# Optimization experiments

Hardware: AMD Instinct MI355X
Metric: run time of the kernel (lower is better)

## Reference

```python
import jax, jax.numpy as jnp
import numpy as np

WINDOW_SIZE = 11
SIGMA = 1.5
C1 = 0.01 ** 2
C2 = 0.03 ** 2


def _gaussian_window(channels):
    coords = jnp.arange(WINDOW_SIZE, dtype=jnp.float32) - WINDOW_SIZE // 2
    g = jnp.exp(-coords ** 2 / (2.0 * SIGMA ** 2))
    g = g / g.sum()
    w2d = g[:, None] * g[None, :]                      # [K, K]
    # depthwise kernel: [out_ch=C, in_ch/groups=1, K, K]
    return jnp.broadcast_to(w2d[None, None], (channels, 1, WINDOW_SIZE, WINDOW_SIZE))


def _depthwise_conv(x, window):
    # x: [B, C, H, W]; grouped conv with feature_group_count = C, SAME padding
    C = x.shape[1]
    pad = WINDOW_SIZE // 2
    return jax.lax.conv_general_dilated(
        x, window,
        window_strides=(1, 1),
        padding=((pad, pad), (pad, pad)),
        dimension_numbers=("NCHW", "OIHW", "NCHW"),
        feature_group_count=C,
    )


def setup_inputs() -> dict:
    key = jax.random.key(0)
    k1, k2 = jax.random.split(key)
    shape = (16, 3, 512, 512)
    pred = jax.random.uniform(k1, shape, dtype=jnp.float32)
    target = jax.random.uniform(k2, shape, dtype=jnp.float32)
    return {"pred": pred, "target": target}


def reference(pred, target):
    C = pred.shape[1]
    window = _gaussian_window(C)
    mu_p = _depthwise_conv(pred, window)
    mu_t = _depthwise_conv(target, window)
    mu_p_sq = mu_p ** 2
    mu_t_sq = mu_t ** 2
    mu_cross = mu_p * mu_t
    sigma_p_sq = _depthwise_conv(pred ** 2, window) - mu_p_sq
    sigma_t_sq = _depthwise_conv(target ** 2, window) - mu_t_sq
    sigma_cross = _depthwise_conv(pred * target, window) - mu_cross
    ssim_map = ((2.0 * mu_cross + C1) * (2.0 * sigma_cross + C2)) / (
        (mu_p_sq + mu_t_sq + C1) * (sigma_p_sq + sigma_t_sq + C2)
    )
    return 1.0 - ssim_map.mean()
```

## Files before the change

### kernel.cpp

```cpp
#include <hip/hip_runtime.h>

#define HH 512
#define WW 512
#define NPLANE 48
#define BY 128
#define CHK 16
#define NCH (BY / CHK)
#define SLOTS 40
#define KS 11

typedef __attribute__((ext_vector_type(8))) short short8;
typedef __attribute__((ext_vector_type(4))) float floatx4;
typedef __attribute__((ext_vector_type(2))) float float2v;
typedef __attribute__((ext_vector_type(2))) __bf16 bf16x2v;

__device__ inline unsigned pk2bf_rne(float a, float b) {
    union { float f; unsigned u; } ua, ub;
    ua.f = a; ub.f = b;
    unsigned lo = (ua.u + 0x7FFFu + ((ua.u >> 16) & 1u)) >> 16;
    unsigned hi = (ub.u + 0x7FFFu + ((ub.u >> 16) & 1u)) >> 16;
    return lo | (hi << 16);
}

__device__ inline unsigned pkbf(float a, float b) {
    float2v f = {a, b};
    bf16x2v v = __builtin_convertvector(f, bf16x2v);
    return __builtin_bit_cast(unsigned, v);
}

struct Raw { float4 p0, p1, t0, t1; };

__global__ __launch_bounds__(256, 4) void ssim_kernel(
    const float* __restrict__ pred, const float* __restrict__ target,
    float* __restrict__ ws_sum)
{
    __shared__ __align__(16) short ring[4][5][16][SLOTS];
    __shared__ float red[4];

    const int tid = threadIdx.x;
    const int wv = tid >> 6;
    const int lane = tid & 63;
    const int m = lane & 15;
    const int quad = lane >> 4;

    float wsum = 0.f;
#pragma unroll
    for (int k = 0; k < KS; ++k) {
        float d = (float)(k - 5);
        wsum += __expf(-d * d * (1.0f / 4.5f));
    }
    const float invs = 1.0f / wsum;

    short8 Wf;
    {
        union { short8 v; unsigned u[4]; } W;
#pragma unroll
        for (int jj = 0; jj < 4; ++jj) {
            float v0, v1;
            {
                int idx = quad * 8 + 2 * jj - m - 3;
                float d = (float)(idx - 5);
                v0 = (idx >= 0 && idx < KS) ? __expf(-d * d * (1.0f / 4.5f)) * invs : 0.f;
            }
            {
                int idx = quad * 8 + 2 * jj + 1 - m - 3;
                float d = (float)(idx - 5);
                v1 = (idx >= 0 && idx < KS) ? __expf(-d * d * (1.0f / 4.5f)) * invs : 0.f;
            }
            W.u[jj] = pk2bf_rne(v0, v1);
        }
        Wf = W.v;
    }

    const size_t poff = (size_t)blockIdx.z * HH * WW;
    const float* __restrict__ pp = pred + poff;
    const float* __restrict__ tp = target + poff;
    const int X0 = blockIdx.x * 64 + wv * 16;
    const int rawX = X0 - 8;
    const int Y0 = blockIdx.y * BY;

    const float C1 = 1.0e-4f;
    const float C2 = 9.0e-4f;
    float lsum = 0.f;
    const floatx4 z = {0.f, 0.f, 0.f, 0.f};

    auto load_raw = [&](int k) -> Raw {
        Raw r;
        r.p0 = make_float4(0, 0, 0, 0); r.p1 = make_float4(0, 0, 0, 0);
        r.t0 = make_float4(0, 0, 0, 0); r.t1 = make_float4(0, 0, 0, 0);
        const int row = Y0 + CHK * k - 8 + m;
        if ((unsigned)row < (unsigned)HH) {
            const float* pr = pp + (size_t)row * WW;
            const float* tr = tp + (size_t)row * WW;
            const int c0 = rawX + quad * 8;
            if ((unsigned)c0 < (unsigned)WW) {
                r.p0 = *(const float4*)(pr + c0);
                r.t0 = *(const float4*)(tr + c0);
            }
            if ((unsigned)(c0 + 4) < (unsigned)WW) {
                r.p1 = *(const float4*)(pr + c0 + 4);
                r.t1 = *(const float4*)(tr + c0 + 4);
            }
        }
        return r;
    };

    auto h_step = [&](const Raw& r, int sb) {
        const float p[8] = {r.p0.x, r.p0.y, r.p0.z, r.p0.w,
                            r.p1.x, r.p1.y, r.p1.z, r.p1.w};
        const float t[8] = {r.t0.x, r.t0.y, r.t0.z, r.t0.w,
                            r.t1.x, r.t1.y, r.t1.z, r.t1.w};
        union { short8 v; unsigned u[4]; } Fp, Ft, Fpp, Ftt, Fpt;
#pragma unroll
        for (int jj = 0; jj < 4; ++jj) {
            const float a0 = p[2 * jj], a1 = p[2 * jj + 1];
            const float b0 = t[2 * jj], b1 = t[2 * jj + 1];
            Fp.u[jj]  = pkbf(a0, a1);
            Ft.u[jj]  = pkbf(b0, b1);
            Fpp.u[jj] = pkbf(a0 * a0, a1 * a1);
            Ftt.u[jj] = pkbf(b0 * b0, b1 * b1);
            Fpt.u[jj] = pkbf(a0 * b0, a1 * b1);
        }
        floatx4 Dp  = __builtin_amdgcn_mfma_f32_16x16x32_bf16(Fp.v,  Wf, z, 0, 0, 0);
        floatx4 Dt  = __builtin_amdgcn_mfma_f32_16x16x32_bf16(Ft.v,  Wf, z, 0, 0, 0);
        floatx4 Dpp = __builtin_amdgcn_mfma_f32_16x16x32_bf16(Fpp.v, Wf, z, 0, 0, 0);
        floatx4 Dtt = __builtin_amdgcn_mfma_f32_16x16x32_bf16(Ftt.v, Wf, z, 0, 0, 0);
        floatx4 Dpt = __builtin_amdgcn_mfma_f32_16x16x32_bf16(Fpt.v, Wf, z, 0, 0, 0);
        int slot = sb + quad * 4;
        if (slot >= SLOTS) slot -= SLOTS;
        uint2 v;
        v.x = pkbf(Dp[0], Dp[1]);   v.y = pkbf(Dp[2], Dp[3]);
        *(uint2*)&ring[wv][0][m][slot] = v;
        v.x = pkbf(Dt[0], Dt[1]);   v.y = pkbf(Dt[2], Dt[3]);
        *(uint2*)&ring[wv][1][m][slot] = v;
        v.x = pkbf(Dpp[0], Dpp[1]); v.y = pkbf(Dpp[2], Dpp[3]);
        *(uint2*)&ring[wv][2][m][slot] = v;
        v.x = pkbf(Dtt[0], Dtt[1]); v.y = pkbf(Dtt[2], Dtt[3]);
        *(uint2*)&ring[wv][3][m][slot] = v;
        v.x = pkbf(Dpt[0], Dpt[1]); v.y = pkbf(Dpt[2], Dpt[3]);
        *(uint2*)&ring[wv][4][m][slot] = v;
    };

    Raw A = load_raw(0);
    Raw B = load_raw(1);
    Raw C = load_raw(2);
    h_step(A, (0 * CHK + SLOTS - 8) % SLOTS);
    h_step(B, (1 * CHK + SLOTS - 8) % SLOTS);
    int hb = (2 * CHK + SLOTS - 8) % SLOTS;
    int vb = SLOTS - 8;
#pragma unroll 1
    for (int i = 0; i < NCH; ++i) {
        int sq = vb + quad * 8;
        if (sq >= SLOTS) sq -= SLOTS;
        const short8 Bp  = *(const short8*)&ring[wv][0][m][sq];
        const short8 Bt  = *(const short8*)&ring[wv][1][m][sq];
        const short8 Bpp = *(const short8*)&ring[wv][2][m][sq];
        const short8 Btt = *(const short8*)&ring[wv][3][m][sq];
        const short8 Bpt = *(const short8*)&ring[wv][4][m][sq];
        vb += CHK; if (vb >= SLOTS) vb -= SLOTS;

        if (i + 2 <= NCH) {
            h_step(C, hb);
            hb += CHK; if (hb >= SLOTS) hb -= SLOTS;
        }
        if (i + 3 <= NCH) C = load_raw(i + 3);

        floatx4 Mp  = __builtin_amdgcn_mfma_f32_16x16x32_bf16(Wf, Bp,  z, 0, 0, 0);
        floatx4 Mt  = __builtin_amdgcn_mfma_f32_16x16x32_bf16(Wf, Bt,  z, 0, 0, 0);
        floatx4 Mpp = __builtin_amdgcn_mfma_f32_16x16x32_bf16(Wf, Bpp, z, 0, 0, 0);
        floatx4 Mtt = __builtin_amdgcn_mfma_f32_16x16x32_bf16(Wf, Btt, z, 0, 0, 0);
        floatx4 Mpt = __builtin_amdgcn_mfma_f32_16x16x32_bf16(Wf, Bpt, z, 0, 0, 0);
#pragma unroll
        for (int r = 0; r < 4; ++r) {
            const float mup = Mp[r], mut = Mt[r];
            const float mupsq = mup * mup, mutsq = mut * mut, mucr = mup * mut;
            const float sp2 = Mpp[r] - mupsq;
            const float st2 = Mtt[r] - mutsq;
            const float scr = Mpt[r] - mucr;
            const float n1 = 2.f * mucr + C1;
            const float n2 = 2.f * scr + C2;
            const float d1 = mupsq + mutsq + C1;
            const float d2 = sp2 + st2 + C2;
            lsum += __fdividef(n1 * n2, d1 * d2);
        }
    }

#pragma unroll
    for (int off = 32; off > 0; off >>= 1) lsum += __shfl_down(lsum, off, 64);
    if (lane == 0) red[wv] = lsum;
    __syncthreads();
    if (tid == 0) {
        atomicAdd(ws_sum, red[0] + red[1] + red[2] + red[3]);
    }
}

__global__ void finalize_kernel(const float* __restrict__ ws_sum,
                                float* __restrict__ out) {
    out[0] = 1.0f - ws_sum[0] * (1.0f / 12582912.0f);
}

extern "C" void kernel_launch(void* const* d_in, const int* in_sizes, int n_in,
                              void* d_out, int out_size, void* d_ws, size_t ws_size,
                              hipStream_t stream) {
    const float* pred = (const float*)d_in[0];
    const float* target = (const float*)d_in[1];
    float* out = (float*)d_out;
    float* ws = (float*)d_ws;

    hipMemsetAsync(ws, 0, sizeof(float), stream);
    dim3 grid(WW / 64, HH / BY, NPLANE);
    ssim_kernel<<<grid, 256, 0, stream>>>(pred, target, ws);
    finalize_kernel<<<1, 1, 0, stream>>>(ws, out);
}
```

Measured before the change: 140.3 us.

## Double rows per block and deepen global-load prefetch with two-way unrolled ring loop

Each block now covers 256 rows instead of 128, which halves the number of blocks and the redundant halo rows loaded per block. The main loop is unrolled by two and alternates between two raw-load registers, so loads are issued two chunks ahead instead of one. Launch bounds drop to 3 blocks per SM to leave registers for the extra in-flight loads. The cost is fewer blocks (768) and lower occupancy, which may hurt latency hiding and load balance across CUs.

```diff
diff --git a/kernel.cpp b/kernel.cpp
--- a/kernel.cpp
+++ b/kernel.cpp
@@ -3,7 +3,7 @@
 #define HH 512
 #define WW 512
 #define NPLANE 48
-#define BY 128
+#define BY 256
 #define CHK 16
 #define NCH (BY / CHK)
 #define SLOTS 40
@@ -30,7 +30,7 @@
 
 struct Raw { float4 p0, p1, t0, t1; };
 
-__global__ __launch_bounds__(256, 4) void ssim_kernel(
+__global__ __launch_bounds__(256, 3) void ssim_kernel(
     const float* __restrict__ pred, const float* __restrict__ target,
     float* __restrict__ ws_sum)
 {
@@ -141,30 +141,7 @@
         *(uint2*)&ring[wv][4][m][slot] = v;
     };
 
-    Raw A = load_raw(0);
-    Raw B = load_raw(1);
-    Raw C = load_raw(2);
-    h_step(A, (0 * CHK + SLOTS - 8) % SLOTS);
-    h_step(B, (1 * CHK + SLOTS - 8) % SLOTS);
-    int hb = (2 * CHK + SLOTS - 8) % SLOTS;
-    int vb = SLOTS - 8;
-#pragma unroll 1
-    for (int i = 0; i < NCH; ++i) {
-        int sq = vb + quad * 8;
-        if (sq >= SLOTS) sq -= SLOTS;
-        const short8 Bp  = *(const short8*)&ring[wv][0][m][sq];
-        const short8 Bt  = *(const short8*)&ring[wv][1][m][sq];
-        const short8 Bpp = *(const short8*)&ring[wv][2][m][sq];
-        const short8 Btt = *(const short8*)&ring[wv][3][m][sq];
-        const short8 Bpt = *(const short8*)&ring[wv][4][m][sq];
-        vb += CHK; if (vb >= SLOTS) vb -= SLOTS;
-
-        if (i + 2 <= NCH) {
-            h_step(C, hb);
-            hb += CHK; if (hb >= SLOTS) hb -= SLOTS;
-        }
-        if (i + 3 <= NCH) C = load_raw(i + 3);
-
+    auto v_tail = [&](short8 Bp, short8 Bt, short8 Bpp, short8 Btt, short8 Bpt) {
         floatx4 Mp  = __builtin_amdgcn_mfma_f32_16x16x32_bf16(Wf, Bp,  z, 0, 0, 0);
         floatx4 Mt  = __builtin_amdgcn_mfma_f32_16x16x32_bf16(Wf, Bt,  z, 0, 0, 0);
         floatx4 Mpp = __builtin_amdgcn_mfma_f32_16x16x32_bf16(Wf, Bpp, z, 0, 0, 0);
@@ -183,6 +160,51 @@
             const float d2 = sp2 + st2 + C2;
             lsum += __fdividef(n1 * n2, d1 * d2);
         }
+    };
+
+    Raw A = load_raw(0);
+    Raw B = load_raw(1);
+    int hb = SLOTS - 8;
+    int vb = SLOTS - 8;
+    h_step(A, hb); hb += CHK; if (hb >= SLOTS) hb -= SLOTS;
+    A = load_raw(2);
+    h_step(B, hb); hb += CHK; if (hb >= SLOTS) hb -= SLOTS;
+    B = load_raw(3);
+
+#pragma unroll 1
+    for (int i = 0; i < NCH; i += 2) {
+        {
+            int sq = vb + quad * 8;
+            if (sq >= SLOTS) sq -= SLOTS;
+            const short8 Bp  = *(const short8*)&ring[wv][0][m][sq];
+            const short8 Bt  = *(const short8*)&ring[wv][1][m][sq];
+            const short8 Bpp = *(const short8*)&ring[wv][2][m][sq];
+            const short8 Btt = *(const short8*)&ring[wv][3][m][sq];
+            const short8 Bpt = *(const short8*)&ring[wv][4][m][sq];
+            vb += CHK; if (vb >= SLOTS) vb -= SLOTS;
+            if (i + 2 <= NCH) {
+                h_step(A, hb);
+                hb += CHK; if (hb >= SLOTS) hb -= SLOTS;
+            }
+            if (i + 4 <= NCH) A = load_raw(i + 4);
+            v_tail(Bp, Bt, Bpp, Btt, Bpt);
+        }
+        {
+            int sq = vb + quad * 8;
+            if (sq >= SLOTS) sq -= SLOTS;
+            const short8 Bp  = *(const short8*)&ring[wv][0][m][sq];
+            const short8 Bt  = *(const short8*)&ring[wv][1][m][sq];
+            const short8 Bpp = *(const short8*)&ring[wv][2][m][sq];
+            const short8 Btt = *(const short8*)&ring[wv][3][m][sq];
+            const short8 Bpt = *(const short8*)&ring[wv][4][m][sq];
+            vb += CHK; if (vb >= SLOTS) vb -= SLOTS;
+            if (i + 3 <= NCH) {
+                h_step(B, hb);
+                hb += CHK; if (hb >= SLOTS) hb -= SLOTS;
+            }
+            if (i + 5 <= NCH) B = load_raw(i + 5);
+            v_tail(Bp, Bt, Bpp, Btt, Bpt);
+        }
     }
 
 #pragma unroll
```

After: 142.1 us. About the same (+1.3%).
